# Performance work log

Hardware: AMD Instinct MI355X
Metric: run time of the kernel (lower is better)

Reference implementation:

```python
import jax, jax.numpy as jnp
import numpy as np

B, N, D = 4096, 64, 512
LN_EPS = 1e-5


def setup_inputs() -> dict:
    key = jax.random.key(0)
    k1, k2 = jax.random.split(key)
    return {
        "embeddings": jax.random.normal(k1, (B, N, D), dtype=jnp.float32),
        "ln_gamma": jnp.ones((D,), dtype=jnp.float32),
        "ln_beta": jnp.zeros((D,), dtype=jnp.float32),
        "Wv": jax.random.normal(k2, (D, 1), dtype=jnp.float32) * (1.0 / np.sqrt(D)),
        "bv": jnp.zeros((1,), dtype=jnp.float32),
    }


def reference(embeddings, ln_gamma, ln_beta, Wv, bv):
    # LayerNorm over last dim
    mu = jnp.mean(embeddings, axis=-1, keepdims=True)
    var = jnp.mean(jnp.square(embeddings - mu), axis=-1, keepdims=True)
    e = (embeddings - mu) * jax.lax.rsqrt(var + LN_EPS) * ln_gamma + ln_beta

    query = e[:, :1, :]          # [B, 1, D]
    key_v = e[:, 1:, :]          # [B, N-1, D] (key == value)

    qk = jnp.tanh(query * key_v)                 # broadcasted elementwise mul + tanh
    scores = (qk @ Wv + bv)[..., 0]              # [B, N-1] tiny D->1 projection
    alphas = jax.nn.softmax(scores, axis=-1)[..., None]  # [B, N-1, 1]

    em_a = alphas * key_v                        # softmax-weighted values
    return jnp.concatenate([query, em_a], axis=-2)  # [B, N, D]
```

## Files before the change

kernel.cpp:

```cpp
#include <hip/hip_runtime.h>
#include <math.h>

#define NROWS 64
#define DCOLS 512
#define HCOL  256
#define BDIM  512
#define NWV   8
#define RPW   8
#define BPB   8

typedef float f32x4 __attribute__((ext_vector_type(4)));

__device__ __forceinline__ void wave_reduce_sum2(float& a, float& b) {
#pragma unroll
    for (int off = 32; off > 0; off >>= 1) {
        a += __shfl_xor(a, off, 64);
        b += __shfl_xor(b, off, 64);
    }
}
__device__ __forceinline__ float wave_reduce_sum(float v) {
#pragma unroll
    for (int off = 32; off > 0; off >>= 1)
        v += __shfl_xor(v, off, 64);
    return v;
}

__device__ __forceinline__ float hsum8(f32x4 a, f32x4 b) {
    return ((a.x + a.y) + (a.z + a.w)) + ((b.x + b.y) + (b.z + b.w));
}
__device__ __forceinline__ float hsumsq8(f32x4 a, f32x4 b) {
    return (a.x*a.x + a.y*a.y + a.z*a.z + a.w*a.w)
         + (b.x*b.x + b.y*b.y + b.z*b.z + b.w*b.w);
}

__device__ __forceinline__ float fast_tanh(float x) {
    float e = __expf(2.0f * x);
    return 1.0f - 2.0f / (e + 1.0f);
}

__device__ __forceinline__ void lds_barrier() {
    asm volatile("s_waitcnt lgkmcnt(0)" ::: "memory");
    __builtin_amdgcn_s_barrier();
}

__device__ __forceinline__ void glds16(const float* g, float* l) {
    __builtin_amdgcn_global_load_lds(
        (const __attribute__((address_space(1))) void*)g,
        (__attribute__((address_space(3)))       void*)l,
        16, 0, 0);
}

__global__ __launch_bounds__(BDIM, 4) void fused_ln_attn_kernel(
    const float* __restrict__ emb,
    const float* __restrict__ gamma,
    const float* __restrict__ beta,
    const float* __restrict__ Wv,
    const float* __restrict__ bv,
    float* __restrict__ out,
    int B)
{
    __shared__ __align__(16) float s_buf[NROWS * HCOL];
    __shared__ __align__(16) float s_q[DCOLS];
    __shared__ __align__(16) float s_g[DCOLS];
    __shared__ __align__(16) float s_b[DCOLS];
    __shared__ __align__(16) float s_w[DCOLS];
    __shared__ float s_den[2][NWV];

    const int tid  = threadIdx.x;
    const int wave = tid >> 6;
    const int lane = tid & 63;
    const int c0   = lane << 2;
    const int c1   = HCOL + c0;
    const int r0   = wave * RPW;

    s_g[tid] = gamma[tid];
    s_b[tid] = beta[tid];
    s_w[tid] = Wv[tid];
    const float bias = bv[0];

    const int bstart = blockIdx.x * BPB;

    f32x4 cx0[RPW];
    {
        const float* eb = emb + (size_t)bstart * (NROWS * DCOLS);
#pragma unroll
        for (int i = 0; i < RPW; ++i) {
            const int r = r0 + i;
            glds16(eb + r * DCOLS + c1, s_buf + r * HCOL);
            cx0[i] = *(const f32x4*)(eb + r * DCOLS + c0);
        }
    }
    asm volatile("s_waitcnt vmcnt(0) lgkmcnt(0)" ::: "memory");
    __builtin_amdgcn_s_barrier();

#pragma unroll 1
    for (int t = 0; t < BPB; ++t) {
        const int bb = bstart + t;
        const float* eb = emb + (size_t)bb * (NROWS * DCOLS);
        float*       ob = out + (size_t)bb * (NROWS * DCOLS);

        asm volatile("s_waitcnt vmcnt(8)" ::: "memory");
        __builtin_amdgcn_sched_barrier(0);

        f32x4 e0[RPW];
        {
            const f32x4 g0 = *(const f32x4*)(s_g + c0);
            const f32x4 g1 = *(const f32x4*)(s_g + c1);
            const f32x4 b0 = *(const f32x4*)(s_b + c0);
            const f32x4 b1 = *(const f32x4*)(s_b + c1);
#pragma unroll
            for (int i = 0; i < RPW; ++i) {
                const int r = r0 + i;
                const f32x4 x0 = cx0[i];
                const f32x4 x1 = *(const f32x4*)(s_buf + r * HCOL + c0);

                float s = hsum8(x0, x1), ss = hsumsq8(x0, x1);
                wave_reduce_sum2(s, ss);

                const float mu  = s * (1.0f / (float)DCOLS);
                const float var = ss * (1.0f / (float)DCOLS) - mu * mu;
                const float rs  = rsqrtf(var + 1e-5f);

                e0[i] = (x0 - mu) * rs * g0 + b0;
                const f32x4 t1 = (x1 - mu) * rs * g1 + b1;
                *(f32x4*)(s_buf + r * HCOL + c0) = t1;

                if (wave == 0 && i == 0) {
                    *(f32x4*)(s_q + c0) = e0[0];
                    *(f32x4*)(s_q + c1) = t1;
                }
            }
        }

        if (t + 1 < BPB) {
            const float* nb = eb + NROWS * DCOLS;
#pragma unroll
            for (int i = 0; i < RPW; ++i)
                cx0[i] = *(const f32x4*)(nb + (r0 + i) * DCOLS + c0);
        }
        __builtin_amdgcn_sched_barrier(0);

        lds_barrier();

        const f32x4 q0 = *(const f32x4*)(s_q + c0);
        const f32x4 q1 = *(const f32x4*)(s_q + c1);
        const f32x4 w0 = *(const f32x4*)(s_w + c0);
        const f32x4 w1 = *(const f32x4*)(s_w + c1);

        float ex[RPW];
        float denw = 0.0f;
#pragma unroll
        for (int i = 0; i < RPW; ++i) {
            const int r = r0 + i;
            const f32x4 t1 = *(const f32x4*)(s_buf + r * HCOL + c0);
            float p;
            p  = fast_tanh(q0.x * e0[i].x) * w0.x;
            p += fast_tanh(q0.y * e0[i].y) * w0.y;
            p += fast_tanh(q0.z * e0[i].z) * w0.z;
            p += fast_tanh(q0.w * e0[i].w) * w0.w;
            p += fast_tanh(q1.x * t1.x) * w1.x;
            p += fast_tanh(q1.y * t1.y) * w1.y;
            p += fast_tanh(q1.z * t1.z) * w1.z;
            p += fast_tanh(q1.w * t1.w) * w1.w;
            const float tot = wave_reduce_sum(p) + bias;
            const float e   = __expf(tot);
            ex[i] = (r == 0) ? 0.0f : e;
            denw += ex[i];
        }
        if (lane == 0) s_den[t & 1][wave] = denw;

        lds_barrier();

        float den = 0.0f;
#pragma unroll
        for (int w = 0; w < NWV; ++w) den += s_den[t & 1][w];
        const float inv = 1.0f / den;

#pragma unroll
        for (int i = 0; i < RPW; ++i) {
            const int r = r0 + i;
            const float a  = (r == 0) ? 1.0f : ex[i] * inv;
            const f32x4 t1 = *(const f32x4*)(s_buf + r * HCOL + c0);
            __builtin_nontemporal_store(t1 * a, (f32x4*)(ob + r * DCOLS + c1));
        }
        asm volatile("s_waitcnt lgkmcnt(0)" ::: "memory");
        __builtin_amdgcn_sched_barrier(0);

        if (t + 1 < BPB) {
            const float* nb = eb + NROWS * DCOLS;
#pragma unroll
            for (int i = 0; i < RPW; ++i)
                glds16(nb + (r0 + i) * DCOLS + c1, s_buf + (r0 + i) * HCOL);
        }
        __builtin_amdgcn_sched_barrier(0);

#pragma unroll
        for (int i = 0; i < RPW; ++i) {
            const int r = r0 + i;
            const float a = (r == 0) ? 1.0f : ex[i] * inv;
            __builtin_nontemporal_store(e0[i] * a, (f32x4*)(ob + r * DCOLS + c0));
        }
    }
}

extern "C" void kernel_launch(void* const* d_in, const int* in_sizes, int n_in,
                              void* d_out, int out_size, void* d_ws, size_t ws_size,
                              hipStream_t stream) {
    const float* emb   = (const float*)d_in[0];
    const float* gamma = (const float*)d_in[1];
    const float* beta  = (const float*)d_in[2];
    const float* Wv    = (const float*)d_in[3];
    const float* bv    = (const float*)d_in[4];
    float* out = (float*)d_out;

    const int B = in_sizes[0] / (NROWS * DCOLS);
    const int grid = (B + BPB - 1) / BPB;
    fused_ln_attn_kernel<<<grid, BDIM, 0, stream>>>(emb, gamma, beta, Wv, bv, out, B);
}
```

Measured before the change: 217.9 us.

## Precompute next query-row LayerNorm into double-buffered LDS to drop a barrier

Wave 0 now normalizes the query row (row 0) of the next batch element one iteration early and writes it into a double-buffered shared query array. This removes the block-wide barrier that used to sit between the LayerNorm phase and the scoring phase. Row 0 is also dropped from the general LN, scoring and glds loops, and its outputs are taken from the shared query buffer instead. The cost is extra code and registers in wave 0 and some imbalance across waves, since wave 0 now does extra query work while handling one fewer regular row.

After: 336.0 us. +54.2%, slower.

```diff
diff --git a/kernel.cpp b/kernel.cpp
--- a/kernel.cpp
+++ b/kernel.cpp
@@ -60,7 +60,7 @@
     int B)
 {
     __shared__ __align__(16) float s_buf[NROWS * HCOL];
-    __shared__ __align__(16) float s_q[DCOLS];
+    __shared__ __align__(16) float s_q[2][DCOLS];
     __shared__ __align__(16) float s_g[DCOLS];
     __shared__ __align__(16) float s_b[DCOLS];
     __shared__ __align__(16) float s_w[DCOLS];
@@ -86,8 +86,23 @@
 #pragma unroll
         for (int i = 0; i < RPW; ++i) {
             const int r = r0 + i;
-            glds16(eb + r * DCOLS + c1, s_buf + r * HCOL);
-            cx0[i] = *(const f32x4*)(eb + r * DCOLS + c0);
+            if (r != 0) {
+                glds16(eb + r * DCOLS + c1, s_buf + r * HCOL);
+                cx0[i] = *(const f32x4*)(eb + r * DCOLS + c0);
+            }
+        }
+        if (wave == 0) {
+            const f32x4 xa = *(const f32x4*)(eb + c0);
+            const f32x4 xb = *(const f32x4*)(eb + c1);
+            float s = hsum8(xa, xb), ss = hsumsq8(xa, xb);
+            wave_reduce_sum2(s, ss);
+            const float mu  = s * (1.0f / (float)DCOLS);
+            const float var = ss * (1.0f / (float)DCOLS) - mu * mu;
+            const float rs  = rsqrtf(var + 1e-5f);
+            *(f32x4*)(&s_q[0][0] + c0) = (xa - mu) * rs * *(const f32x4*)(s_g + c0)
+                                         + *(const f32x4*)(s_b + c0);
+            *(f32x4*)(&s_q[0][0] + c1) = (xb - mu) * rs * *(const f32x4*)(s_g + c1)
+                                         + *(const f32x4*)(s_b + c1);
         }
     }
     asm volatile("s_waitcnt vmcnt(0) lgkmcnt(0)" ::: "memory");
@@ -102,48 +117,50 @@
         asm volatile("s_waitcnt vmcnt(8)" ::: "memory");
         __builtin_amdgcn_sched_barrier(0);
 
+        const f32x4 g0 = *(const f32x4*)(s_g + c0);
+        const f32x4 g1 = *(const f32x4*)(s_g + c1);
+        const f32x4 b0 = *(const f32x4*)(s_b + c0);
+        const f32x4 b1 = *(const f32x4*)(s_b + c1);
+
         f32x4 e0[RPW];
-        {
-            const f32x4 g0 = *(const f32x4*)(s_g + c0);
-            const f32x4 g1 = *(const f32x4*)(s_g + c1);
-            const f32x4 b0 = *(const f32x4*)(s_b + c0);
-            const f32x4 b1 = *(const f32x4*)(s_b + c1);
+#pragma unroll
+        for (int i = 0; i < RPW; ++i) {
+            const int r = r0 + i;
+            if (r == 0) continue;
+            const f32x4 x0 = cx0[i];
+            const f32x4 x1 = *(const f32x4*)(s_buf + r * HCOL + c0);
+
+            float s = hsum8(x0, x1), ss = hsumsq8(x0, x1);
+            wave_reduce_sum2(s, ss);
+
+            const float mu  = s * (1.0f / (float)DCOLS);
+            const float var = ss * (1.0f / (float)DCOLS) - mu * mu;
+            const float rs  = rsqrtf(var + 1e-5f);
+
+            e0[i] = (x0 - mu) * rs * g0 + b0;
+            const f32x4 t1 = (x1 - mu) * rs * g1 + b1;
+            *(f32x4*)(s_buf + r * HCOL + c0) = t1;
+        }
+
+        f32x4 qxa, qxb;
+        if (wave == 0 && t + 1 < BPB) {
+            const float* nb = eb + NROWS * DCOLS;
+            qxa = *(const f32x4*)(nb + c0);
+            qxb = *(const f32x4*)(nb + c1);
+        }
+
+        if (t + 1 < BPB) {
+            const float* nb = eb + NROWS * DCOLS;
 #pragma unroll
             for (int i = 0; i < RPW; ++i) {
                 const int r = r0 + i;
-                const f32x4 x0 = cx0[i];
-                const f32x4 x1 = *(const f32x4*)(s_buf + r * HCOL + c0);
-
-                float s = hsum8(x0, x1), ss = hsumsq8(x0, x1);
-                wave_reduce_sum2(s, ss);
-
-                const float mu  = s * (1.0f / (float)DCOLS);
-                const float var = ss * (1.0f / (float)DCOLS) - mu * mu;
-                const float rs  = rsqrtf(var + 1e-5f);
-
-                e0[i] = (x0 - mu) * rs * g0 + b0;
-                const f32x4 t1 = (x1 - mu) * rs * g1 + b1;
-                *(f32x4*)(s_buf + r * HCOL + c0) = t1;
-
-                if (wave == 0 && i == 0) {
-                    *(f32x4*)(s_q + c0) = e0[0];
-                    *(f32x4*)(s_q + c1) = t1;
-                }
+                if (r != 0) cx0[i] = *(const f32x4*)(nb + r * DCOLS + c0);
             }
         }
-
-        if (t + 1 < BPB) {
-            const float* nb = eb + NROWS * DCOLS;
-#pragma unroll
-            for (int i = 0; i < RPW; ++i)
-                cx0[i] = *(const f32x4*)(nb + (r0 + i) * DCOLS + c0);
-        }
-        __builtin_amdgcn_sched_barrier(0);
-
-        lds_barrier();
-
-        const f32x4 q0 = *(const f32x4*)(s_q + c0);
-        const f32x4 q1 = *(const f32x4*)(s_q + c1);
+        __builtin_amdgcn_sched_barrier(0);
+
+        const f32x4 q0 = *(const f32x4*)(&s_q[t & 1][0] + c0);
+        const f32x4 q1 = *(const f32x4*)(&s_q[t & 1][0] + c1);
         const f32x4 w0 = *(const f32x4*)(s_w + c0);
         const f32x4 w1 = *(const f32x4*)(s_w + c1);
 
@@ -152,6 +169,7 @@
 #pragma unroll
         for (int i = 0; i < RPW; ++i) {
             const int r = r0 + i;
+            if (r == 0) { ex[i] = 0.0f; continue; }
             const f32x4 t1 = *(const f32x4*)(s_buf + r * HCOL + c0);
             float p;
             p  = fast_tanh(q0.x * e0[i].x) * w0.x;
@@ -163,11 +181,20 @@
             p += fast_tanh(q1.z * t1.z) * w1.z;
             p += fast_tanh(q1.w * t1.w) * w1.w;
             const float tot = wave_reduce_sum(p) + bias;
-            const float e   = __expf(tot);
-            ex[i] = (r == 0) ? 0.0f : e;
+            ex[i] = __expf(tot);
             denw += ex[i];
         }
         if (lane == 0) s_den[t & 1][wave] = denw;
+
+        if (wave == 0 && t + 1 < BPB) {
+            float s = hsum8(qxa, qxb), ss = hsumsq8(qxa, qxb);
+            wave_reduce_sum2(s, ss);
+            const float mu  = s * (1.0f / (float)DCOLS);
+            const float var = ss * (1.0f / (float)DCOLS) - mu * mu;
+            const float rs  = rsqrtf(var + 1e-5f);
+            *(f32x4*)(&s_q[(t + 1) & 1][0] + c0) = (qxa - mu) * rs * g0 + b0;
+            *(f32x4*)(&s_q[(t + 1) & 1][0] + c1) = (qxb - mu) * rs * g1 + b1;
+        }
 
         lds_barrier();
 
@@ -180,7 +207,8 @@
         for (int i = 0; i < RPW; ++i) {
             const int r = r0 + i;
             const float a  = (r == 0) ? 1.0f : ex[i] * inv;
-            const f32x4 t1 = *(const f32x4*)(s_buf + r * HCOL + c0);
+            const f32x4 t1 = (r == 0) ? *(const f32x4*)(&s_q[t & 1][0] + c1)
+                                      : *(const f32x4*)(s_buf + r * HCOL + c0);
             __builtin_nontemporal_store(t1 * a, (f32x4*)(ob + r * DCOLS + c1));
         }
         asm volatile("s_waitcnt lgkmcnt(0)" ::: "memory");
@@ -189,16 +217,20 @@
         if (t + 1 < BPB) {
             const float* nb = eb + NROWS * DCOLS;
 #pragma unroll
-            for (int i = 0; i < RPW; ++i)
-                glds16(nb + (r0 + i) * DCOLS + c1, s_buf + (r0 + i) * HCOL);
-        }
-        __builtin_amdgcn_sched_barrier(0);
-
-#pragma unroll
-        for (int i = 0; i < RPW; ++i) {
-            const int r = r0 + i;
-            const float a = (r == 0) ? 1.0f : ex[i] * inv;
-            __builtin_nontemporal_store(e0[i] * a, (f32x4*)(ob + r * DCOLS + c0));
+            for (int i = 0; i < RPW; ++i) {
+                const int r = r0 + i;
+                if (r != 0) glds16(nb + r * DCOLS + c1, s_buf + r * HCOL);
+            }
+        }
+        __builtin_amdgcn_sched_barrier(0);
+
+#pragma unroll
+        for (int i = 0; i < RPW; ++i) {
+            const int r = r0 + i;
+            const float a  = (r == 0) ? 1.0f : ex[i] * inv;
+            const f32x4 v0 = (r == 0) ? *(const f32x4*)(&s_q[t & 1][0] + c0)
+                                      : e0[i];
+            __builtin_nontemporal_store(v0 * a, (f32x4*)(ob + r * DCOLS + c0));
         }
     }
 }
```
